# Optimization experiments

Measured on AMD Instinct MI355X. Metric: run time of the kernel, lower is better.

## Reference

```python
import jax, jax.numpy as jnp
import numpy as np
import math

B, S, D, H, HD = 2, 2048, 2048, 16, 128
ROPE_THETA = 10000.0


def _rope_cache(seq_len, dim, base, dtype=jnp.float32):
    inv_freq = 1.0 / (base ** (jnp.arange(0, dim, 2, dtype=jnp.float32) / dim))
    t = jnp.arange(seq_len, dtype=jnp.float32)
    freqs = jnp.einsum('i,j->ij', t, inv_freq)          # [S, dim/2]
    emb = jnp.concatenate([freqs, freqs], axis=-1)       # [S, dim]
    return jnp.cos(emb).astype(dtype), jnp.sin(emb).astype(dtype)


def _rotate_half(x):
    x1, x2 = x[..., : x.shape[-1] // 2], x[..., x.shape[-1] // 2:]
    return jnp.concatenate([-x2, x1], axis=-1)


def setup_inputs() -> dict:
    key = jax.random.key(0)
    ks = jax.random.split(key, 6)
    hidden_states = jax.random.normal(ks[0], (B, S, D), dtype=jnp.float32) * 0.02
    w_scale = 1.0 / math.sqrt(D)
    Wq = jax.random.normal(ks[1], (D, D), dtype=jnp.float32) * w_scale
    Wk = jax.random.normal(ks[2], (D, D), dtype=jnp.float32) * w_scale
    Wv = jax.random.normal(ks[3], (D, D), dtype=jnp.float32) * w_scale
    Wo = jax.random.normal(ks[4], (D, D), dtype=jnp.float32) * w_scale
    # additive causal mask [B, 1, S, S]: 0 on/below diag, large negative above
    causal = jnp.tril(jnp.ones((S, S), dtype=bool))
    attention_mask = jnp.where(causal, 0.0, -1e9).astype(jnp.float32)
    attention_mask = jnp.broadcast_to(attention_mask[None, None], (B, 1, S, S))
    position_ids = jnp.broadcast_to(jnp.arange(S, dtype=jnp.int32)[None], (B, S))
    return {
        'hidden_states': hidden_states,
        'attention_mask': attention_mask,
        'position_ids': position_ids,
        'Wq': Wq, 'Wk': Wk, 'Wv': Wv, 'Wo': Wo,
    }


def reference(hidden_states, attention_mask, position_ids, Wq, Wk, Wv, Wo):
    bsz, q_len, _ = hidden_states.shape
    # projections (torch Linear: x @ W.T), then split heads -> [B, H, S, HD]
    def proj(W):
        return jnp.einsum('bsd,ed->bse', hidden_states, W).reshape(bsz, q_len, H, HD).transpose(0, 2, 1, 3)
    q, k, v = proj(Wq), proj(Wk), proj(Wv)
    cos_c, sin_c = _rope_cache(q_len, HD, ROPE_THETA, hidden_states.dtype)
    cos = cos_c[position_ids][:, None]  # [B, 1, S, HD]
    sin = sin_c[position_ids][:, None]
    q = q * cos + _rotate_half(q) * sin
    k = k * cos + _rotate_half(k) * sin
    scores = jnp.einsum('bhqd,bhkd->bhqk', q, k) / math.sqrt(HD)
    scores = scores + attention_mask
    attn_weights = jax.nn.softmax(scores.astype(jnp.float32), axis=-1).astype(q.dtype)
    attn_out = jnp.einsum('bhqk,bhkd->bhqd', attn_weights, v)
    attn_out = attn_out.transpose(0, 2, 1, 3).reshape(bsz, q_len, D)
    out = jnp.einsum('bsd,ed->bse', attn_out, Wo)
    return out
```

## Files before the change

kernel.cpp:

```cpp
#include <hip/hip_runtime.h>

typedef __bf16 bf16;
typedef __bf16 bf16x8 __attribute__((ext_vector_type(8)));
typedef float f32x4 __attribute__((ext_vector_type(4)));

#define D_MODEL 2048
#define SEQ 2048
#define NH 16
#define HEAD_DIM 128
#define NBATCH 2
#define SM_SCALE 0.08838834764831845f
#define WSEG 4194304
#define NT_TILES 32

typedef __attribute__((address_space(1))) const void* gas_cp;
typedef __attribute__((address_space(3))) void* las_p;
__device__ __forceinline__ void ll16(const bf16* g, bf16* l) {
  __builtin_amdgcn_global_load_lds((gas_cp)g, (las_p)l, 16, 0, 0);
}

__device__ __forceinline__ bf16x8 cvt8(const float* p) {
  float4 a = *(const float4*)p;
  float4 b = *(const float4*)(p + 4);
  bf16x8 v;
  v[0] = (bf16)a.x; v[1] = (bf16)a.y; v[2] = (bf16)a.z; v[3] = (bf16)a.w;
  v[4] = (bf16)b.x; v[5] = (bf16)b.y; v[6] = (bf16)b.z; v[7] = (bf16)b.w;
  return v;
}

__global__ __launch_bounds__(256)
void cvt_hidden(const float* __restrict__ src, bf16* __restrict__ dst) {
  size_t i = ((size_t)blockIdx.x * 256 + threadIdx.x) * 8;
  *(bf16x8*)(dst + i) = cvt8(src + i);
}

__global__ __launch_bounds__(256)
void cvt_weights(const float* __restrict__ w0, const float* __restrict__ w1,
                 const float* __restrict__ w2, const float* __restrict__ w3,
                 bf16* __restrict__ dst) {
  const float* src = (blockIdx.y == 0) ? w0 : (blockIdx.y == 1) ? w1
                   : (blockIdx.y == 2) ? w2 : w3;
  size_t i = ((size_t)blockIdx.x * 256 + threadIdx.x) * 8;
  *(bf16x8*)(dst + (size_t)blockIdx.y * WSEG + i) = cvt8(src + i);
}

#define PHASE_SYNC_PRE()                                                     \
  __builtin_amdgcn_s_barrier();                                              \
  asm volatile("s_waitcnt lgkmcnt(0)" ::: "memory");                         \
  __builtin_amdgcn_sched_barrier(0);                                         \
  __builtin_amdgcn_s_setprio(1);

#define PHASE_SYNC_POST()                                                    \
  __builtin_amdgcn_s_setprio(0);                                             \
  __builtin_amdgcn_s_barrier();

template <typename TC, int MODE, int NBN>
__global__ __launch_bounds__(512, 2)
void gemm128(const bf16* __restrict__ A, const bf16* __restrict__ W,
             TC* __restrict__ C, bf16* __restrict__ Qo, bf16* __restrict__ Ko,
             bf16* __restrict__ Vo, const int* __restrict__ pos_ids) {
  __shared__ __align__(16) char smem[147456];

  const int tid  = threadIdx.x;
  const int lane = tid & 63;
  const int w    = tid >> 6;
  const int quad = lane >> 4, l15 = lane & 15;
  const int l8   = lane >> 3, l7 = lane & 7;
  const int kelem = 8 * (l7 ^ l8);
  const int wm = w >> 2;
  const int wn = w & 3;
  const int hh = wn >> 1;
  const int cb = (wn & 1) * 32;

  const int nwg = 32 * NBN;
  const int bid = blockIdx.x;
  const int lin = (bid & 7) * (nwg >> 3) + (bid >> 3);
  const int by = lin / NBN, bx = lin % NBN;
  const int mBase = by << 7, nBase = bx << 8;

  const int kx0 = (quad * 16) ^ ((l15 & 7) << 4);
  const int kx1 = kx0 ^ 64;
  const int arow = wm * 64 + l15;
  const int rb0 = hh * 128 + cb + l15;
  const int rb1 = rb0 + 16, rb2 = rb0 + 64, rb3 = rb0 + 80;

  f32x4 acc[4][4];
#pragma unroll
  for (int i = 0; i < 4; i++)
#pragma unroll
    for (int j = 0; j < 4; j++) acc[i][j] = 0.0f;

  bf16x8 af[4], bfr[4];

#define ST1(GP, ROW0, KT, LB)                                                \
  ll16((GP) + (size_t)((ROW0) + w * 8 + l8) * D_MODEL + (KT) * 64 + kelem,   \
       (bf16*)((LB) + w * 1024));

  {
    char* s0 = smem;
    char* s1 = smem + 49152;
    ST1(A, mBase,       0, s0 + 0);
    ST1(A, mBase + 64,  0, s0 + 8192);
    ST1(W, nBase,       0, s0 + 16384);
    ST1(W, nBase + 64,  0, s0 + 24576);
    ST1(W, nBase + 128, 0, s0 + 32768);
    ST1(W, nBase + 192, 0, s0 + 40960);
    ST1(A, mBase,       1, s1 + 0);
    ST1(A, mBase + 64,  1, s1 + 8192);
    ST1(W, nBase,       1, s1 + 16384);
    ST1(W, nBase + 64,  1, s1 + 24576);
    ST1(W, nBase + 128, 1, s1 + 32768);
    ST1(W, nBase + 192, 1, s1 + 40960);
  }
  asm volatile("s_waitcnt vmcnt(6)" ::: "memory");
  __builtin_amdgcn_s_barrier();

  int buf = 0;
  for (int t = 0; t < NT_TILES; ++t) {
    char* const Sb = smem + buf * 49152;
    const int  pb  = (buf + 2 >= 3) ? buf - 1 : buf + 2;
    char* const Pb = smem + pb * 49152;
    const bool pf  = (t + 2 < NT_TILES);

#pragma unroll
    for (int mi = 0; mi < 4; mi++)
      af[mi] = *(const bf16x8*)(Sb + ((arow + mi * 16) << 7) + kx0);
    bfr[0] = *(const bf16x8*)(Sb + 16384 + (rb0 << 7) + kx0);
    bfr[1] = *(const bf16x8*)(Sb + 16384 + (rb1 << 7) + kx0);
    bfr[2] = *(const bf16x8*)(Sb + 16384 + (rb2 << 7) + kx0);
    bfr[3] = *(const bf16x8*)(Sb + 16384 + (rb3 << 7) + kx0);
    if (pf) {
      ST1(A, mBase,      t + 2, Pb + 0);
      ST1(A, mBase + 64, t + 2, Pb + 8192);
      ST1(W, nBase,      t + 2, Pb + 16384);
    }
    PHASE_SYNC_PRE();
#pragma unroll
    for (int mi = 0; mi < 4; mi++)
#pragma unroll
      for (int ni = 0; ni < 4; ni++)
        acc[mi][ni] = __builtin_amdgcn_mfma_f32_16x16x32_bf16(
            af[mi], bfr[ni], acc[mi][ni], 0, 0, 0);
    PHASE_SYNC_POST();

#pragma unroll
    for (int mi = 0; mi < 4; mi++)
      af[mi] = *(const bf16x8*)(Sb + ((arow + mi * 16) << 7) + kx1);
    bfr[0] = *(const bf16x8*)(Sb + 16384 + (rb0 << 7) + kx1);
    bfr[1] = *(const bf16x8*)(Sb + 16384 + (rb1 << 7) + kx1);
    bfr[2] = *(const bf16x8*)(Sb + 16384 + (rb2 << 7) + kx1);
    bfr[3] = *(const bf16x8*)(Sb + 16384 + (rb3 << 7) + kx1);
    if (pf) {
      ST1(W, nBase + 64,  t + 2, Pb + 24576);
      ST1(W, nBase + 128, t + 2, Pb + 32768);
      ST1(W, nBase + 192, t + 2, Pb + 40960);
    }
    __builtin_amdgcn_s_barrier();
    asm volatile("s_waitcnt lgkmcnt(0)" ::: "memory");
    __builtin_amdgcn_sched_barrier(0);
    __builtin_amdgcn_s_setprio(1);
#pragma unroll
    for (int mi = 0; mi < 4; mi++)
#pragma unroll
      for (int ni = 0; ni < 4; ni++)
        acc[mi][ni] = __builtin_amdgcn_mfma_f32_16x16x32_bf16(
            af[mi], bfr[ni], acc[mi][ni], 0, 0, 0);
    __builtin_amdgcn_s_setprio(0);
    if (pf)
      asm volatile("s_waitcnt vmcnt(6)" ::: "memory");
    else
      asm volatile("s_waitcnt vmcnt(0)" ::: "memory");
    __builtin_amdgcn_s_barrier();

    buf = (buf == 2) ? 0 : buf + 1;
  }
#undef ST1

  if (MODE == 0) {
#pragma unroll
    for (int mi = 0; mi < 4; mi++) {
      const int m = mBase + wm * 64 + mi * 16 + quad * 4;
#pragma unroll
      for (int ni = 0; ni < 4; ni++) {
        const int n = nBase + hh * 128 + cb + (ni & 1) * 16 + (ni >> 1) * 64 + l15;
        TC* cp = C + (size_t)m * D_MODEL + n;
#pragma unroll
        for (int r = 0; r < 4; r++) cp[(size_t)r * D_MODEL] = (TC)acc[mi][ni][r];
      }
    }
  } else {
    const int matrix = nBase >> 11;
    const int nb     = nBase & 2047;
    if (matrix == 2) {
      const int h = (nb >> 7) + hh;
#pragma unroll
      for (int mi = 0; mi < 4; mi++)
#pragma unroll
        for (int ni = 0; ni < 4; ni++) {
          const int hd = cb + (ni & 1) * 16 + (ni >> 1) * 64 + l15;
#pragma unroll
          for (int r = 0; r < 4; r++) {
            int m = mBase + wm * 64 + mi * 16 + quad * 4 + r;
            int b = m >> 11, s2 = m & 2047;
            Vo[((size_t)((b * NH + h) * HEAD_DIM + hd)) * SEQ + s2] =
                (bf16)acc[mi][ni][r];
          }
        }
    } else {
      bf16* Out = (matrix == 0) ? Qo : Ko;
      float invf[2];
#pragma unroll
      for (int ni = 0; ni < 2; ni++)
        invf[ni] = __expf(-(float)(cb + ni * 16 + l15) *
                          (9.210340371976184f / 64.0f));
#pragma unroll
      for (int mi = 0; mi < 4; mi++)
#pragma unroll
        for (int r = 0; r < 4; r++) {
          int m = mBase + wm * 64 + mi * 16 + quad * 4 + r;
          float pos = (float)pos_ids[m];
          bf16* op = Out + (size_t)m * D_MODEL + nb + hh * 128 + cb + l15;
#pragma unroll
          for (int ni = 0; ni < 2; ni++) {
            float sn, cs;
            __sincosf(pos * invf[ni], &sn, &cs);
            float q0 = acc[mi][ni][r];
            float q1 = acc[mi][ni + 2][r];
            op[ni * 16]      = (bf16)(q0 * cs - q1 * sn);
            op[ni * 16 + 64] = (bf16)(q1 * cs + q0 * sn);
          }
        }
    }
  }
}

__global__ __launch_bounds__(256, 3)
void attn_mfma(const bf16* __restrict__ Q, const bf16* __restrict__ K,
               const bf16* __restrict__ Vt, bf16* __restrict__ O) {
  __shared__ __align__(16) bf16 K_lds[64 * 136];
  __shared__ __align__(16) bf16 V_lds[128 * 72];
  __shared__ __align__(16) bf16 P_lds[64 * 72];

  const int tid  = threadIdx.x;
  const int lane = tid & 63;
  const int w    = tid >> 6;
  const int quad = lane >> 4, l15 = lane & 15;
  const int s    = 31 - blockIdx.y;
  const int bh   = blockIdx.x;
  const size_t qkBase = (size_t)(bh >> 4) * SEQ * D_MODEL + (size_t)(bh & 15) * HEAD_DIM;
  const size_t vBase  = (size_t)bh * HEAD_DIM * SEQ;

  const int qbase = s * 64 + w * 16;

  bf16x8 qa[4];
#pragma unroll
  for (int kk = 0; kk < 4; kk++)
    qa[kk] = *(const bf16x8*)(Q + qkBase + (size_t)(qbase + l15) * D_MODEL + kk * 32 + quad * 8);

  bf16x8 ones;
#pragma unroll
  for (int i = 0; i < 8; i++) ones[i] = (bf16)1.0f;

  f32x4 oacc[8], ls;
#pragma unroll
  for (int ni = 0; ni < 8; ni++) oacc[ni] = 0.0f;
  ls = 0.0f;

  const int ntiles = s + 1;

  bf16x8 kr[4], vr[4];
  auto loadKV = [&](int t0) {
#pragma unroll
    for (int i = 0; i < 4; i++) {
      int c = tid + 256 * i;
      kr[i] = *(const bf16x8*)(K + qkBase + (size_t)(t0 + (c >> 4)) * D_MODEL + (c & 15) * 8);
    }
#pragma unroll
    for (int i = 0; i < 4; i++) {
      int c = tid + 256 * i;
      vr[i] = *(const bf16x8*)(Vt + vBase + (size_t)(c >> 3) * SEQ + t0 + (c & 7) * 8);
    }
  };
  loadKV(0);

  const int prow = w * 16;

  for (int tt = 0; tt < ntiles; tt++) {
    const int t0 = tt * 64;
    __syncthreads();
#pragma unroll
    for (int i = 0; i < 4; i++) {
      int c = tid + 256 * i;
      *(bf16x8*)&K_lds[(c >> 4) * 136 + (c & 15) * 8] = kr[i];
    }
#pragma unroll
    for (int i = 0; i < 4; i++) {
      int c = tid + 256 * i;
      *(bf16x8*)&V_lds[(c >> 3) * 72 + (c & 7) * 8] = vr[i];
    }
    __syncthreads();
    if (tt + 1 < ntiles) loadKV(t0 + 64);

    f32x4 sacc[4];
#pragma unroll
    for (int ni = 0; ni < 4; ni++) sacc[ni] = 0.0f;
#pragma unroll
    for (int kk = 0; kk < 4; kk++) {
#pragma unroll
      for (int ni = 0; ni < 4; ni++) {
        bf16x8 kf = *(const bf16x8*)&K_lds[(ni * 16 + l15) * 136 + kk * 32 + quad * 8];
        sacc[ni] = __builtin_amdgcn_mfma_f32_16x16x32_bf16(qa[kk], kf, sacc[ni], 0, 0, 0);
      }
    }

    if (tt == s) {
#pragma unroll
      for (int r = 0; r < 4; r++) {
        int qrow = qbase + quad * 4 + r;
#pragma unroll
        for (int ni = 0; ni < 4; ni++) {
          int tcol = t0 + ni * 16 + l15;
          float pv = (tcol <= qrow) ? __expf(fminf(sacc[ni][r] * SM_SCALE, 30.0f)) : 0.0f;
          P_lds[(prow + quad * 4 + r) * 72 + ni * 16 + l15] = (bf16)pv;
        }
      }
    } else {
#pragma unroll
      for (int r = 0; r < 4; r++)
#pragma unroll
        for (int ni = 0; ni < 4; ni++)
          P_lds[(prow + quad * 4 + r) * 72 + ni * 16 + l15] =
              (bf16)__expf(fminf(sacc[ni][r] * SM_SCALE, 30.0f));
    }

#pragma unroll
    for (int kk2 = 0; kk2 < 2; kk2++) {
      bf16x8 pf = *(const bf16x8*)&P_lds[(prow + l15) * 72 + kk2 * 32 + quad * 8];
#pragma unroll
      for (int ni = 0; ni < 8; ni++) {
        bf16x8 vf = *(const bf16x8*)&V_lds[(ni * 16 + l15) * 72 + kk2 * 32 + quad * 8];
        oacc[ni] = __builtin_amdgcn_mfma_f32_16x16x32_bf16(pf, vf, oacc[ni], 0, 0, 0);
      }
      ls = __builtin_amdgcn_mfma_f32_16x16x32_bf16(pf, ones, ls, 0, 0, 0);
    }
  }

#pragma unroll
  for (int r = 0; r < 4; r++) {
    float inv = 1.0f / ls[r];
    bf16* op = O + qkBase + (size_t)(qbase + quad * 4 + r) * D_MODEL;
#pragma unroll
    for (int ni = 0; ni < 8; ni++)
      op[ni * 16 + l15] = (bf16)(oacc[ni][r] * inv);
  }
}

extern "C" void kernel_launch(void* const* d_in, const int* in_sizes, int n_in,
                              void* d_out, int out_size, void* d_ws, size_t ws_size,
                              hipStream_t stream) {
  const float* hidden = (const float*)d_in[0];
  const int* pos = (const int*)d_in[2];
  const float* Wq = (const float*)d_in[3];
  const float* Wk = (const float*)d_in[4];
  const float* Wv = (const float*)d_in[5];
  const float* Wo = (const float*)d_in[6];
  float* out = (float*)d_out;

  const size_t TENS = (size_t)NBATCH * SEQ * D_MODEL;
  bf16* Qb = (bf16*)d_ws;
  bf16* Kb = Qb + TENS;
  bf16* Vt = Kb + TENS;
  bf16* AO = Vt + TENS;
  bf16* Hb = AO + TENS;
  bf16* Wb = Hb + TENS;

  cvt_hidden<<<dim3(TENS / 2048), dim3(256), 0, stream>>>(hidden, Hb);
  cvt_weights<<<dim3(WSEG / 2048, 4), dim3(256), 0, stream>>>(Wq, Wk, Wv, Wo, Wb);

  gemm128<bf16, 1, 24><<<dim3(768), dim3(512), 0, stream>>>(
      Hb, Wb, (bf16*)nullptr, Qb, Kb, Vt, pos);

  attn_mfma<<<dim3(NBATCH * NH, 32), dim3(256), 0, stream>>>(Qb, Kb, Vt, AO);

  gemm128<float, 0, 8><<<dim3(256), dim3(512), 0, stream>>>(
      AO, Wb + 3 * (size_t)WSEG, out, nullptr, nullptr, nullptr, nullptr);
}
```

Baseline: 382.0 us.

## Double-buffer LDS fragments in GEMM so reads overlap MFMA of previous half

Measured after the change: 364.6 us. 1.05x faster.

```diff
diff --git a/kernel.cpp b/kernel.cpp
--- a/kernel.cpp
+++ b/kernel.cpp
@@ -44,15 +44,23 @@
   *(bf16x8*)(dst + (size_t)blockIdx.y * WSEG + i) = cvt8(src + i);
 }
 
-#define PHASE_SYNC_PRE()                                                     \
-  __builtin_amdgcn_s_barrier();                                              \
-  asm volatile("s_waitcnt lgkmcnt(0)" ::: "memory");                         \
-  __builtin_amdgcn_sched_barrier(0);                                         \
-  __builtin_amdgcn_s_setprio(1);
-
-#define PHASE_SYNC_POST()                                                    \
-  __builtin_amdgcn_s_setprio(0);                                             \
-  __builtin_amdgcn_s_barrier();
+#define LDFRAG(DA, DB, SB, KX)                                               \
+  _Pragma("unroll") for (int mi = 0; mi < 4; mi++)                           \
+      DA[mi] = *(const bf16x8*)((SB) + ((arow + mi * 16) << 7) + (KX));      \
+  DB[0] = *(const bf16x8*)((SB) + 16384 + (rb0 << 7) + (KX));                \
+  DB[1] = *(const bf16x8*)((SB) + 16384 + (rb1 << 7) + (KX));                \
+  DB[2] = *(const bf16x8*)((SB) + 16384 + (rb2 << 7) + (KX));                \
+  DB[3] = *(const bf16x8*)((SB) + 16384 + (rb3 << 7) + (KX));
+
+#define MMAC(AF, BF)                                                         \
+  _Pragma("unroll") for (int mi = 0; mi < 4; mi++)                           \
+  _Pragma("unroll") for (int ni = 0; ni < 4; ni++)                           \
+      acc[mi][ni] = __builtin_amdgcn_mfma_f32_16x16x32_bf16(                 \
+          AF[mi], BF[ni], acc[mi][ni], 0, 0, 0);
+
+#define ST1(GP, ROW0, KT, LB)                                                \
+  ll16((GP) + (size_t)((ROW0) + w * 8 + l8) * D_MODEL + (KT) * 64 + kelem,   \
+       (bf16*)((LB) + w * 1024));
 
 template <typename TC, int MODE, int NBN>
 __global__ __launch_bounds__(512, 2)
@@ -90,11 +98,8 @@
 #pragma unroll
     for (int j = 0; j < 4; j++) acc[i][j] = 0.0f;
 
-  bf16x8 af[4], bfr[4];
-
-#define ST1(GP, ROW0, KT, LB)                                                \
-  ll16((GP) + (size_t)((ROW0) + w * 8 + l8) * D_MODEL + (KT) * 64 + kelem,   \
-       (bf16*)((LB) + w * 1024));
+  bf16x8 aP[4], bP[4];
+  bf16x8 aQ[4], bQ[4];
 
   {
     char* s0 = smem;
@@ -114,67 +119,51 @@
   }
   asm volatile("s_waitcnt vmcnt(6)" ::: "memory");
   __builtin_amdgcn_s_barrier();
+  LDFRAG(aP, bP, smem, kx0);
 
   int buf = 0;
   for (int t = 0; t < NT_TILES; ++t) {
-    char* const Sb = smem + buf * 49152;
-    const int  pb  = (buf + 2 >= 3) ? buf - 1 : buf + 2;
-    char* const Pb = smem + pb * 49152;
-    const bool pf  = (t + 2 < NT_TILES);
-
-#pragma unroll
-    for (int mi = 0; mi < 4; mi++)
-      af[mi] = *(const bf16x8*)(Sb + ((arow + mi * 16) << 7) + kx0);
-    bfr[0] = *(const bf16x8*)(Sb + 16384 + (rb0 << 7) + kx0);
-    bfr[1] = *(const bf16x8*)(Sb + 16384 + (rb1 << 7) + kx0);
-    bfr[2] = *(const bf16x8*)(Sb + 16384 + (rb2 << 7) + kx0);
-    bfr[3] = *(const bf16x8*)(Sb + 16384 + (rb3 << 7) + kx0);
+    char* const Sb  = smem + buf * 49152;
+    const int  nb1  = (buf + 1 == 3) ? 0 : buf + 1;
+    const int  pb   = (buf + 2 >= 3) ? buf - 1 : buf + 2;
+    char* const Nb  = smem + nb1 * 49152;
+    char* const Pb  = smem + pb * 49152;
+    const bool pf   = (t + 2 < NT_TILES);
+
+    LDFRAG(aQ, bQ, Sb, kx1);
     if (pf) {
       ST1(A, mBase,      t + 2, Pb + 0);
       ST1(A, mBase + 64, t + 2, Pb + 8192);
       ST1(W, nBase,      t + 2, Pb + 16384);
     }
-    PHASE_SYNC_PRE();
-#pragma unroll
-    for (int mi = 0; mi < 4; mi++)
-#pragma unroll
-      for (int ni = 0; ni < 4; ni++)
-        acc[mi][ni] = __builtin_amdgcn_mfma_f32_16x16x32_bf16(
-            af[mi], bfr[ni], acc[mi][ni], 0, 0, 0);
-    PHASE_SYNC_POST();
-
-#pragma unroll
-    for (int mi = 0; mi < 4; mi++)
-      af[mi] = *(const bf16x8*)(Sb + ((arow + mi * 16) << 7) + kx1);
-    bfr[0] = *(const bf16x8*)(Sb + 16384 + (rb0 << 7) + kx1);
-    bfr[1] = *(const bf16x8*)(Sb + 16384 + (rb1 << 7) + kx1);
-    bfr[2] = *(const bf16x8*)(Sb + 16384 + (rb2 << 7) + kx1);
-    bfr[3] = *(const bf16x8*)(Sb + 16384 + (rb3 << 7) + kx1);
+    __builtin_amdgcn_sched_barrier(0);
+    __builtin_amdgcn_s_setprio(1);
+    MMAC(aP, bP);
+    __builtin_amdgcn_s_setprio(0);
+    asm volatile("s_waitcnt lgkmcnt(0)" ::: "memory");
+    if (pf)
+      asm volatile("s_waitcnt vmcnt(3)" ::: "memory");
+    else
+      asm volatile("s_waitcnt vmcnt(0)" ::: "memory");
+    __builtin_amdgcn_s_barrier();
+
+    if (t + 1 < NT_TILES) {
+      LDFRAG(aP, bP, Nb, kx0);
+    }
     if (pf) {
       ST1(W, nBase + 64,  t + 2, Pb + 24576);
       ST1(W, nBase + 128, t + 2, Pb + 32768);
       ST1(W, nBase + 192, t + 2, Pb + 40960);
     }
-    __builtin_amdgcn_s_barrier();
-    asm volatile("s_waitcnt lgkmcnt(0)" ::: "memory");
     __builtin_amdgcn_sched_barrier(0);
     __builtin_amdgcn_s_setprio(1);
-#pragma unroll
-    for (int mi = 0; mi < 4; mi++)
-#pragma unroll
-      for (int ni = 0; ni < 4; ni++)
-        acc[mi][ni] = __builtin_amdgcn_mfma_f32_16x16x32_bf16(
-            af[mi], bfr[ni], acc[mi][ni], 0, 0, 0);
+    MMAC(aQ, bQ);
     __builtin_amdgcn_s_setprio(0);
-    if (pf)
-      asm volatile("s_waitcnt vmcnt(6)" ::: "memory");
-    else
-      asm volatile("s_waitcnt vmcnt(0)" ::: "memory");
+    asm volatile("s_waitcnt lgkmcnt(0)" ::: "memory");
     __builtin_amdgcn_s_barrier();
 
-    buf = (buf == 2) ? 0 : buf + 1;
-  }
-#undef ST1
+    buf = nb1;
+  }
 
   if (MODE == 0) {
 #pragma unroll
```
